# Performance work log

Hardware: AMD Instinct MI355X
Metric: run time of the kernel (lower is better)

The kernel has to match this reference:

```python
import jax, jax.numpy as jnp
import numpy as np

NEG_SLOPE = 0.01  # torch leaky_relu default

def _lrelu(x):
    return jax.nn.leaky_relu(x, NEG_SLOPE)

def _l2norm(x, axis):
    # torch F.normalize(p=2, eps=1e-12)
    n = jnp.linalg.norm(x, axis=axis, keepdims=True)
    return x / jnp.maximum(n, 1e-12)

def setup_inputs() -> dict:
    key = jax.random.key(0)
    ks = jax.random.split(key, 12)
    Nda, Nq, C, Din, Dout = 10000, 64, 1024, 128, 256
    target_adj = (jax.random.uniform(ks[0], (Nda, Nda)) < 0.002).astype(jnp.float32)
    query_adj = (jax.random.uniform(ks[1], (Nq, Nq)) < 0.2).astype(jnp.float32)
    node_features_da = jax.random.normal(ks[2], (Nda, Din), dtype=jnp.float32)
    node_features_q = jax.random.normal(ks[3], (Nq, Din), dtype=jnp.float32)
    candidate_set = jax.random.randint(ks[4], (C,), 0, Nda)
    candidate_adj = (jax.random.uniform(ks[5], (C, C)) < 0.01).astype(jnp.float32)
    s_in = 1.0 / np.sqrt(Din).astype(np.float32)
    s_out = 1.0 / np.sqrt(Dout).astype(np.float32)
    W1_da = jax.random.normal(ks[6], (Din, Dout), dtype=jnp.float32) * s_in
    W1_q = jax.random.normal(ks[7], (Din, Dout), dtype=jnp.float32) * s_in
    W2_da = jax.random.normal(ks[8], (Dout, Dout), dtype=jnp.float32) * s_out
    W2_q = jax.random.normal(ks[9], (Dout, Dout), dtype=jnp.float32) * s_out
    threshold = jnp.float32(0.2)
    return {"target_adj": target_adj, "node_features_da": node_features_da,
            "query_adj": query_adj, "node_features_q": node_features_q,
            "candidate_set": candidate_set, "candidate_adj": candidate_adj,
            "threshold": threshold, "W1_da": W1_da, "W1_q": W1_q,
            "W2_da": W2_da, "W2_q": W2_q}

def _cross_cosine(q, da, candidate_set):
    # cosine similarity between each query node and each candidate target node: [Nq, C]
    return _l2norm(q, 1) @ _l2norm(da[candidate_set], 1).T

def reference(target_adj, node_features_da, query_adj, node_features_q,
              candidate_set, candidate_adj, threshold, W1_da, W1_q, W2_da, W2_q):
    # layer 1: GCN propagation on both graphs (gcn(adj,x) = adj @ x @ W)
    da1 = _lrelu(target_adj @ (node_features_da @ W1_da))   # [Nda, D]
    q1 = _lrelu(query_adj @ (node_features_q @ W1_q))       # [Nq, D]
    c1 = _cross_cosine(q1, da1, candidate_set)               # [Nq, C]
    pre_da1 = da1[candidate_set]                             # [C, D]
    # NOTE: da1[candidate_set].data = ... mutates a temporary in torch -> no-op on da1
    att_da1 = _lrelu(da1)                                    # dropout in eval = identity
    h1_q = c1 @ pre_da1                                      # [Nq, D]
    att_q1 = _lrelu(q1 + _l2norm(h1_q, 0))
    # layer 2
    da2 = _lrelu(target_adj @ (att_da1 @ W2_da))
    q2 = _lrelu(query_adj @ (att_q1 @ W2_q))
    c2 = _cross_cosine(q2, da2, candidate_set)
    pre_da2 = da2[candidate_set]
    att_da2 = _lrelu(da2)                                    # in-place update is again a no-op
    h2_q = c2 @ pre_da2
    att_q2 = _lrelu(q2 + _l2norm(h2_q, 0))
    # graph-level matching score per target node
    emb = jnp.mean(att_q2, axis=0, keepdims=True)            # [1, D]
    num = att_da2 @ emb[0]                                   # [Nda]
    den = jnp.maximum(jnp.linalg.norm(att_da2, axis=1) * jnp.linalg.norm(emb), 1e-8)
    end = (num / den)[None, :]                               # [1, Nda]
    # threshold selection expressed with a mask (jit-safe, same math: excluded
    # rows/cols are zero and do not affect L2 norms, sums, or the trace)
    m = (end[0] > threshold).astype(att_da2.dtype)           # [Nda]
    F_ = att_da2 * m[:, None]
    re_adj = F_ @ F_.T                                       # [Nda, Nda]
    nor_re = _l2norm(re_adj, 1) * target_adj                 # elementwise with original adj
    cnt = jnp.sum(m)
    total = jnp.sum(nor_re)
    tr = jnp.trace(nor_re)
    has = cnt > 0
    pre_avg_degree = jnp.where(has, total / jnp.maximum(cnt, 1.0), 0.0)
    pre_avg_nodes = jnp.where(has, tr, 0.0)
    pre_density = jnp.where(has, 2.0 * total / (tr * (tr - 1.0) + 1e-4), 0.0)
    return (end, att_da2, att_q2, pre_avg_degree, pre_density, pre_avg_nodes)
```

## Files before the change

### kernel.cpp

```cpp
#include <hip/hip_runtime.h>

constexpr int NDA = 10000;
constexpr int NQ  = 64;
constexpr int CND = 1024;
constexpr int DIN = 128;
constexpr int D   = 256;
constexpr int CAP = 96;
constexpr int NB64 = ((NDA + 63) / 64) * (D / 64);
constexpr int GCHUNK = 400;

#define LRELU(x) ((x) >= 0.f ? (x) : 0.01f * (x))

__device__ __forceinline__ float wave_red64(float v) {
#pragma unroll
    for (int o = 32; o; o >>= 1) v += __shfl_down(v, o);
    return v;
}

struct GemmSmem  { float As[32][65]; float Bs[32][68]; };
struct CrossSmem { float qs[D]; float cmw[256]; int sci[256]; float red[4]; float sqn; float part[4][256]; };
struct SpmmSmem  { int sc[CAP]; float part[4][256]; };
struct CsrSmem   { int scnt; };
struct EndSmem   { float se[D]; float scnt; float red[4]; };
struct FinalSmem { int sc[CAP]; float part[4][256]; int n; int sdiag; float r1[4], r2[4], r3[4]; };
struct Attq4Smem { float hbuf[64][65]; float red[4][64]; float invs[64]; };

template <bool RELU_A, bool RELU_C>
__device__ __forceinline__ void gemm_body(GemmSmem& sm, int bx, int by,
                                          const float* __restrict__ A,
                                          const float* __restrict__ B,
                                          float* __restrict__ C,
                                          int M, int N, int K) {
    const int bm = bx * 64, bn = by * 64;
    const int tid = threadIdx.x;
    const int tx = tid & 15, ty = tid >> 4;
    const int lm = tid >> 2, lk = (tid & 3) * 8;
    const int kb = tid >> 3, nb = (tid & 7) * 8;
    const bool aValid = (bm + lm) < M;
    const float* aPtr = A + (size_t)(bm + lm) * K + lk;
    const float* bPtr = B + (size_t)kb * N + bn + nb;
    float4 ra0 = make_float4(0.f, 0.f, 0.f, 0.f), ra1 = ra0, rb0, rb1;
    if (aValid) { ra0 = *(const float4*)aPtr; ra1 = *(const float4*)(aPtr + 4); }
    rb0 = *(const float4*)bPtr;
    rb1 = *(const float4*)(bPtr + 4);
    float acc[4][4] = {};
    for (int k0 = 0; k0 < K; k0 += 32) {
        float4 wa0 = ra0, wa1 = ra1, wb0 = rb0, wb1 = rb1;
        if (RELU_A) {
            wa0.x = LRELU(wa0.x); wa0.y = LRELU(wa0.y); wa0.z = LRELU(wa0.z); wa0.w = LRELU(wa0.w);
            wa1.x = LRELU(wa1.x); wa1.y = LRELU(wa1.y); wa1.z = LRELU(wa1.z); wa1.w = LRELU(wa1.w);
        }
        sm.As[lk + 0][lm] = wa0.x; sm.As[lk + 1][lm] = wa0.y;
        sm.As[lk + 2][lm] = wa0.z; sm.As[lk + 3][lm] = wa0.w;
        sm.As[lk + 4][lm] = wa1.x; sm.As[lk + 5][lm] = wa1.y;
        sm.As[lk + 6][lm] = wa1.z; sm.As[lk + 7][lm] = wa1.w;
        *(float4*)&sm.Bs[kb][nb]     = wb0;
        *(float4*)&sm.Bs[kb][nb + 4] = wb1;
        __syncthreads();
        if (k0 + 32 < K) {
            if (aValid) {
                ra0 = *(const float4*)(aPtr + k0 + 32);
                ra1 = *(const float4*)(aPtr + k0 + 36);
            }
            rb0 = *(const float4*)(bPtr + (size_t)(k0 + 32) * N);
            rb1 = *(const float4*)(bPtr + (size_t)(k0 + 32) * N + 4);
        }
#pragma unroll
        for (int kk = 0; kk < 32; kk++) {
            float av[4], bv[4];
#pragma unroll
            for (int i = 0; i < 4; i++) av[i] = sm.As[kk][ty * 4 + i];
#pragma unroll
            for (int j = 0; j < 4; j++) bv[j] = sm.Bs[kk][tx * 4 + j];
#pragma unroll
            for (int i = 0; i < 4; i++)
#pragma unroll
                for (int j = 0; j < 4; j++) acc[i][j] += av[i] * bv[j];
        }
        __syncthreads();
    }
#pragma unroll
    for (int i = 0; i < 4; i++) {
        int r = bm + ty * 4 + i;
        if (r < M) {
            float4 v = make_float4(acc[i][0], acc[i][1], acc[i][2], acc[i][3]);
            if (RELU_C) { v.x = LRELU(v.x); v.y = LRELU(v.y); v.z = LRELU(v.z); v.w = LRELU(v.w); }
            *(float4*)(C + (size_t)r * N + bn + tx * 4) = v;
        }
    }
}

__device__ __forceinline__ void csr_body(CsrSmem& sm, const float* __restrict__ adj,
                                         int* __restrict__ cols,
                                         int* __restrict__ rowcnt, int row) {
    if (threadIdx.x == 0) sm.scnt = 0;
    __syncthreads();
    const float4* rp = (const float4*)(adj + (size_t)row * NDA);
    for (int i = threadIdx.x; i < NDA / 4; i += 256) {
        float4 v = rp[i];
        if (v.x != 0.f) { int s = atomicAdd(&sm.scnt, 1); if (s < CAP) cols[row * CAP + s] = 4 * i; }
        if (v.y != 0.f) { int s = atomicAdd(&sm.scnt, 1); if (s < CAP) cols[row * CAP + s] = 4 * i + 1; }
        if (v.z != 0.f) { int s = atomicAdd(&sm.scnt, 1); if (s < CAP) cols[row * CAP + s] = 4 * i + 2; }
        if (v.w != 0.f) { int s = atomicAdd(&sm.scnt, 1); if (s < CAP) cols[row * CAP + s] = 4 * i + 3; }
    }
    __syncthreads();
    if (threadIdx.x == 0) rowcnt[row] = min(sm.scnt, CAP);
}

__device__ __forceinline__ void spmm_body(SpmmSmem& sm, const int* __restrict__ cols,
                                          const int* __restrict__ rowcnt,
                                          const float* __restrict__ X,
                                          float* __restrict__ out1,
                                          float* __restrict__ out2, int row) {
    int t = threadIdx.x;
    int w = t >> 6, lane = t & 63;
    int cnt = rowcnt[row];
    if (t < cnt) sm.sc[t] = cols[row * CAP + t];
    __syncthreads();
    float4 acc = make_float4(0.f, 0.f, 0.f, 0.f);
    int k = w;
    for (; k + 4 < cnt; k += 8) {
        const float4* x0 = (const float4*)(X + (size_t)sm.sc[k] * D);
        const float4* x1 = (const float4*)(X + (size_t)sm.sc[k + 4] * D);
        float4 v0 = x0[lane];
        float4 v1 = x1[lane];
        acc.x += v0.x + v1.x; acc.y += v0.y + v1.y;
        acc.z += v0.z + v1.z; acc.w += v0.w + v1.w;
    }
    for (; k < cnt; k += 4) {
        const float4* x0 = (const float4*)(X + (size_t)sm.sc[k] * D);
        float4 v0 = x0[lane];
        acc.x += v0.x; acc.y += v0.y; acc.z += v0.z; acc.w += v0.w;
    }
    *(float4*)&sm.part[w][lane * 4] = acc;
    __syncthreads();
    float s = sm.part[0][t] + sm.part[1][t] + sm.part[2][t] + sm.part[3][t];
    float v = LRELU(s);
    out1[(size_t)row * D + t] = v;
    if (out2) out2[(size_t)row * D + t] = LRELU(v);
}

__device__ __forceinline__ void cross_body(CrossSmem& sm, const float* __restrict__ q,
                                           const float* __restrict__ da,
                                           const int* __restrict__ cand,
                                           float* __restrict__ hpart,
                                           int r, int qr) {
    int t = threadIdx.x;
    int w = t >> 6, lane = t & 63;
    float qv = q[r * D + t];
    sm.qs[t] = qv;
    sm.sci[t] = cand[qr * 256 + t];
    float p = wave_red64(qv * qv);
    if (lane == 0) sm.red[w] = p;
    __syncthreads();
    if (t == 0) sm.sqn = fmaxf(sqrtf(sm.red[0] + sm.red[1] + sm.red[2] + sm.red[3]), 1e-12f);
    __syncthreads();
    float qn = sm.sqn;
    float4 qv4 = *(const float4*)&sm.qs[lane * 4];
    for (int c = w * 64; c < w * 64 + 64; c++) {
        const float4* rp = (const float4*)(da + (size_t)sm.sci[c] * D);
        float4 v = rp[lane];
        float dp = qv4.x * v.x + qv4.y * v.y + qv4.z * v.z + qv4.w * v.w;
        float sq = v.x * v.x + v.y * v.y + v.z * v.z + v.w * v.w;
#pragma unroll
        for (int o = 32; o; o >>= 1) { dp += __shfl_down(dp, o); sq += __shfl_down(sq, o); }
        if (lane == 0) sm.cmw[c] = dp / (qn * fmaxf(sqrtf(sq), 1e-12f));
    }
    __syncthreads();
    float4 acc = make_float4(0.f, 0.f, 0.f, 0.f);
    for (int c = w; c < 256; c += 8) {
        float w0 = sm.cmw[c], w1 = sm.cmw[c + 4];
        const float4* p0 = (const float4*)(da + (size_t)sm.sci[c] * D);
        const float4* p1 = (const float4*)(da + (size_t)sm.sci[c + 4] * D);
        float4 v0 = p0[lane];
        float4 v1 = p1[lane];
        acc.x += w0 * v0.x + w1 * v1.x;
        acc.y += w0 * v0.y + w1 * v1.y;
        acc.z += w0 * v0.z + w1 * v1.z;
        acc.w += w0 * v0.w + w1 * v1.w;
    }
    *(float4*)&sm.part[w][lane * 4] = acc;
    __syncthreads();
    float hs = sm.part[0][t] + sm.part[1][t] + sm.part[2][t] + sm.part[3][t];
    hpart[((size_t)qr * NQ + r) * D + t] = hs;
}

__global__ __launch_bounds__(256) void stage0_kernel(const float* __restrict__ adj,
                                                     int* __restrict__ cols,
                                                     int* __restrict__ rowcnt,
                                                     const float* __restrict__ Fda,
                                                     const float* __restrict__ W1da,
                                                     float* __restrict__ X1,
                                                     const float* __restrict__ Fq,
                                                     const float* __restrict__ W1q,
                                                     float* __restrict__ Xq,
                                                     float* __restrict__ G) {
    __shared__ union { GemmSmem g; CsrSmem z; } sm;
    int bid = blockIdx.x;
    if (bid < NB64) {
        gemm_body<false, false>(sm.g, bid >> 2, bid & 3, Fda, W1da, X1, NDA, D, DIN);
    } else if (bid < NB64 + 4) {
        gemm_body<false, false>(sm.g, 0, bid - NB64, Fq, W1q, Xq, NQ, D, DIN);
    } else if (bid < NB64 + 20) {
        int zb = bid - (NB64 + 4);
        float4* g4 = (float4*)G;
        int base = zb * 1024 + threadIdx.x;
#pragma unroll
        for (int k = 0; k < 4; k++)
            g4[base + k * 256] = make_float4(0.f, 0.f, 0.f, 0.f);
    } else {
        csr_body(sm.z, adj, cols, rowcnt, bid - (NB64 + 20));
    }
}

__global__ __launch_bounds__(256) void stage_sg_kernel(const int* __restrict__ cols,
                                                       const int* __restrict__ rowcnt,
                                                       const float* __restrict__ X,
                                                       float* __restrict__ out1,
                                                       float* __restrict__ out2,
                                                       const float* __restrict__ Aq,
                                                       const float* __restrict__ Bq,
                                                       float* __restrict__ Cq) {
    __shared__ union { GemmSmem g; SpmmSmem s; } sm;
    int bid = blockIdx.x;
    if (bid < 4) {
        gemm_body<false, true>(sm.g, 0, bid, Aq, Bq, Cq, NQ, D, NQ);
    } else {
        spmm_body(sm.s, cols, rowcnt, X, out1, out2, bid - 4);
    }
}

__global__ __launch_bounds__(256) void mergeA_kernel(const float* __restrict__ q1,
                                                     const float* __restrict__ da1,
                                                     const int* __restrict__ cand,
                                                     float* __restrict__ hpart,
                                                     const float* __restrict__ W2da,
                                                     float* __restrict__ Y2) {
    __shared__ union { CrossSmem c; GemmSmem g; } sm;
    int bid = blockIdx.x;
    if (bid < 256) {
        cross_body(sm.c, q1, da1, cand, hpart, bid >> 2, bid & 3);
    } else {
        int t = bid - 256;
        gemm_body<true, false>(sm.g, t >> 2, t & 3, da1, W2da, Y2, NDA, D, D);
    }
}

__global__ __launch_bounds__(256) void cross_kernel(const float* __restrict__ q,
                                                    const float* __restrict__ da,
                                                    const int* __restrict__ cand,
                                                    float* __restrict__ hpart) {
    __shared__ CrossSmem sm;
    cross_body(sm, q, da, cand, hpart, blockIdx.x, blockIdx.y);
}

__global__ __launch_bounds__(256) void qfused_kernel(const float* __restrict__ q,
                                                     const float* __restrict__ hpart,
                                                     const float* __restrict__ W2q,
                                                     float* __restrict__ Zq) {
    __shared__ float aqT[D][65];
    __shared__ float Bs[32][68];
    int d = threadIdx.x;
    float hv[NQ];
    float ss = 0.f;
#pragma unroll
    for (int r = 0; r < NQ; r++) {
        float h = hpart[(size_t)r * D + d]
                + hpart[(size_t)(NQ + r) * D + d]
                + hpart[(size_t)(2 * NQ + r) * D + d]
                + hpart[(size_t)(3 * NQ + r) * D + d];
        hv[r] = h;
        ss += h * h;
    }
    float inv = 1.f / fmaxf(sqrtf(ss), 1e-12f);
#pragma unroll
    for (int r = 0; r < NQ; r++) {
        float v = q[r * D + d] + hv[r] * inv;
        aqT[d][r] = LRELU(v);
    }
    __syncthreads();
    const int bn = blockIdx.x * 64;
    const int tx = d & 15, ty = d >> 4;
    const int kb = d >> 3, nb = (d & 7) * 8;
    float acc[4][4] = {};
    for (int k0 = 0; k0 < D; k0 += 32) {
        float4 b0 = *(const float4*)(W2q + (size_t)(k0 + kb) * D + bn + nb);
        float4 b1 = *(const float4*)(W2q + (size_t)(k0 + kb) * D + bn + nb + 4);
        *(float4*)&Bs[kb][nb]     = b0;
        *(float4*)&Bs[kb][nb + 4] = b1;
        __syncthreads();
#pragma unroll
        for (int kk = 0; kk < 32; kk++) {
            float av[4], bv[4];
#pragma unroll
            for (int i = 0; i < 4; i++) av[i] = aqT[k0 + kk][ty * 4 + i];
#pragma unroll
            for (int j = 0; j < 4; j++) bv[j] = Bs[kk][tx * 4 + j];
#pragma unroll
            for (int i = 0; i < 4; i++)
#pragma unroll
                for (int j = 0; j < 4; j++) acc[i][j] += av[i] * bv[j];
        }
        __syncthreads();
    }
#pragma unroll
    for (int i = 0; i < 4; i++) {
        float4 v = make_float4(acc[i][0], acc[i][1], acc[i][2], acc[i][3]);
        *(float4*)(Zq + (size_t)(ty * 4 + i) * D + bn + tx * 4) = v;
    }
}

__global__ __launch_bounds__(256) void attq4_kernel(const float* __restrict__ q,
                                                    const float* __restrict__ hpart,
                                                    float* __restrict__ attq,
                                                    float* __restrict__ emb,
                                                    float* __restrict__ cnt,
                                                    double* __restrict__ tot,
                                                    double* __restrict__ tr) {
    __shared__ Attq4Smem sm;
    int b = blockIdx.x, t = threadIdx.x;
    int lc = t & 63, rq = t >> 6;
    int c = b * 64 + lc;
    if (b == 0 && t == 0) { *cnt = 0.f; *tot = 0.0; *tr = 0.0; }
    float ss = 0.f;
#pragma unroll
    for (int rr = 0; rr < 16; rr++) {
        int r = rq * 16 + rr;
        float h = hpart[(size_t)r * D + c]
                + hpart[(size_t)(NQ + r) * D + c]
                + hpart[(size_t)(2 * NQ + r) * D + c]
                + hpart[(size_t)(3 * NQ + r) * D + c];
        sm.hbuf[r][lc] = h;
        ss += h * h;
    }
    sm.red[rq][lc] = ss;
    __syncthreads();
    if (rq == 0) {
        float s = sm.red[0][lc] + sm.red[1][lc] + sm.red[2][lc] + sm.red[3][lc];
        sm.invs[lc] = 1.f / fmaxf(sqrtf(s), 1e-12f);
    }
    __syncthreads();
    float inv = sm.invs[lc];
    float es = 0.f;
#pragma unroll
    for (int rr = 0; rr < 16; rr++) {
        int r = rq * 16 + rr;
        float v = q[r * D + c] + sm.hbuf[r][lc] * inv;
        v = LRELU(v);
        attq[r * D + c] = v;
        es += v;
    }
    __syncthreads();
    sm.red[rq][lc] = es;
    __syncthreads();
    if (rq == 0) {
        float e = (sm.red[0][lc] + sm.red[1][lc] + sm.red[2][lc] + sm.red[3][lc]) * (1.f / (float)NQ);
        emb[c] = e;
    }
}

__global__ __launch_bounds__(256) void end_kernel(const float* __restrict__ A,
                                                  const float* __restrict__ emb,
                                                  const float* __restrict__ thr_p,
                                                  float* __restrict__ endv,
                                                  float* __restrict__ m,
                                                  float* __restrict__ cnt) {
    __shared__ EndSmem sm;
    int d = threadIdx.x;
    float ev = emb[d];
    sm.se[d] = ev;
    if (d == 0) sm.scnt = 0.f;
    int w = d >> 6, lane = d & 63;
    float pe = wave_red64(ev * ev);
    if (lane == 0) sm.red[w] = pe;
    __syncthreads();
    float embn = sqrtf(sm.red[0] + sm.red[1] + sm.red[2] + sm.red[3]);
    float thr = *thr_p;
    int row = blockIdx.x * 4 + w;
    const float* ar = A + (size_t)row * D;
    float num = 0.f, sq = 0.f;
#pragma unroll
    for (int s = 0; s < 4; s++) {
        float v = ar[lane + 64 * s];
        num += v * sm.se[lane + 64 * s];
        sq += v * v;
    }
#pragma unroll
    for (int o = 32; o; o >>= 1) { num += __shfl_down(num, o); sq += __shfl_down(sq, o); }
    if (lane == 0) {
        float den = fmaxf(sqrtf(sq) * embn, 1e-8f);
        float e = num / den;
        endv[row] = e;
        float mv = e > thr ? 1.f : 0.f;
        m[row] = mv;
        if (mv != 0.f) atomicAdd(&sm.scnt, 1.f);
    }
    __syncthreads();
    if (d == 0 && sm.scnt != 0.f) atomicAdd(cnt, sm.scnt);
}

__global__ __launch_bounds__(256) void G_kernel(const float* __restrict__ A,
                                                const float* __restrict__ m,
                                                float* __restrict__ G) {
    __shared__ float SA[8][64], SB[8][64];
    int ti = blockIdx.x >> 2, tj = blockIdx.x & 3;
    int base = blockIdx.y * GCHUNK;
    int tid = threadIdx.x;
    int tx = tid & 15, ty = tid >> 4;
    float acc[4][4] = {};
    for (int g0 = 0; g0 < GCHUNK; g0 += 8) {
        for (int l = tid; l < 512; l += 256) {
            int rr = l >> 6, c = l & 63;
            int r = base + g0 + rr;
            float mv = m[r];
            SA[rr][c] = A[(size_t)r * D + ti * 64 + c] * mv;
            SB[rr][c] = A[(size_t)r * D + tj * 64 + c];
        }
        __syncthreads();
#pragma unroll
        for (int rr = 0; rr < 8; rr++) {
            float av[4], bv[4];
#pragma unroll
            for (int i = 0; i < 4; i++) av[i] = SA[rr][ty * 4 + i];
#pragma unroll
            for (int j = 0; j < 4; j++) bv[j] = SB[rr][tx * 4 + j];
#pragma unroll
            for (int i = 0; i < 4; i++)
#pragma unroll
                for (int j = 0; j < 4; j++) acc[i][j] += av[i] * bv[j];
        }
        __syncthreads();
    }
#pragma unroll
    for (int i = 0; i < 4; i++)
#pragma unroll
        for (int j = 0; j < 4; j++)
            atomicAdd(&G[(ti * 64 + ty * 4 + i) * D + tj * 64 + tx * 4 + j], acc[i][j]);
}

__global__ __launch_bounds__(256) void gemmH_kernel(const float* __restrict__ A,
                                                    const float* __restrict__ B,
                                                    float* __restrict__ C) {
    __shared__ GemmSmem sm;
    gemm_body<false, false>(sm, blockIdx.x, blockIdx.y, A, B, C, NDA, D, D);
}

__global__ __launch_bounds__(256) void final_kernel(const int* __restrict__ cols,
                                                    const int* __restrict__ rowcnt,
                                                    const float* __restrict__ m,
                                                    const float* __restrict__ A,
                                                    const float* __restrict__ H,
                                                    double* __restrict__ total,
                                                    double* __restrict__ tr) {
    int i = blockIdx.x;
    if (m[i] == 0.f) return;
    __shared__ FinalSmem sm;
    int t = threadIdx.x;
    int w = t >> 6, lane = t & 63;
    int cnt = rowcnt[i];
    if (t == 0) { sm.n = 0; sm.sdiag = 0; }
    __syncthreads();
    if (t < cnt) {
        int j = cols[i * CAP + t];
        if (m[j] != 0.f) {
            int s = atomicAdd(&sm.n, 1);
            sm.sc[s] = j;
            if (j == i) sm.sdiag = 1;
        }
    }
    __syncthreads();
    int n = sm.n;
    float4 acc = make_float4(0.f, 0.f, 0.f, 0.f);
    int k = w;
    for (; k + 4 < n; k += 8) {
        const float4* x0 = (const float4*)(A + (size_t)sm.sc[k] * D);
        const float4* x1 = (const float4*)(A + (size_t)sm.sc[k + 4] * D);
        float4 v0 = x0[lane];
        float4 v1 = x1[lane];
        acc.x += v0.x + v1.x; acc.y += v0.y + v1.y;
        acc.z += v0.z + v1.z; acc.w += v0.w + v1.w;
    }
    for (; k < n; k += 4) {
        const float4* x0 = (const float4*)(A + (size_t)sm.sc[k] * D);
        float4 v0 = x0[lane];
        acc.x += v0.x; acc.y += v0.y; acc.z += v0.z; acc.w += v0.w;
    }
    *(float4*)&sm.part[w][lane * 4] = acc;
    __syncthreads();
    float av = A[(size_t)i * D + t];
    float hv = H[(size_t)i * D + t];
    float sd = sm.part[0][t] + sm.part[1][t] + sm.part[2][t] + sm.part[3][t];
    float p1 = av * sd, p2 = av * hv, p3 = av * av;
#pragma unroll
    for (int o = 32; o; o >>= 1) {
        p1 += __shfl_down(p1, o);
        p2 += __shfl_down(p2, o);
        p3 += __shfl_down(p3, o);
    }
    if (lane == 0) { sm.r1[w] = p1; sm.r2[w] = p2; sm.r3[w] = p3; }
    __syncthreads();
    if (t == 0) {
        float num  = sm.r1[0] + sm.r1[1] + sm.r1[2] + sm.r1[3];
        float den2 = sm.r2[0] + sm.r2[1] + sm.r2[2] + sm.r2[3];
        float self = sm.r3[0] + sm.r3[1] + sm.r3[2] + sm.r3[3];
        float denom = fmaxf(sqrtf(den2), 1e-12f);
        double inv = 1.0 / (double)denom;
        if (num != 0.f) atomicAdd(total, (double)num * inv);
        if (sm.sdiag) atomicAdd(tr, (double)self * inv);
    }
}

__global__ void scalars_kernel(const float* __restrict__ cnt,
                               const double* __restrict__ total,
                               const double* __restrict__ tr,
                               float* __restrict__ out) {
    float c = *cnt;
    float T = (float)*total;
    float R = (float)*tr;
    bool has = c > 0.f;
    out[0] = has ? (T / fmaxf(c, 1.f)) : 0.f;
    out[1] = has ? (2.f * T / (R * (R - 1.f) + 1e-4f)) : 0.f;
    out[2] = has ? R : 0.f;
}

extern "C" void kernel_launch(void* const* d_in, const int* in_sizes, int n_in,
                              void* d_out, int out_size, void* d_ws, size_t ws_size,
                              hipStream_t stream) {
    (void)in_sizes; (void)n_in; (void)out_size; (void)ws_size;
    const float* adj  = (const float*)d_in[0];
    const float* Fda  = (const float*)d_in[1];
    const float* Qadj = (const float*)d_in[2];
    const float* Fq   = (const float*)d_in[3];
    const int*   cand = (const int*)d_in[4];
    const float* thr  = (const float*)d_in[6];
    const float* W1da = (const float*)d_in[7];
    const float* W1q  = (const float*)d_in[8];
    const float* W2da = (const float*)d_in[9];
    const float* W2q  = (const float*)d_in[10];

    float* out = (float*)d_out;
    float* o_end    = out;
    float* o_attda2 = out + NDA;
    float* o_attq2  = out + NDA + (size_t)NDA * D;
    float* o_sc     = o_attq2 + NQ * D;

    char* w = (char*)d_ws;
    size_t off = 0;
    auto alloc = [&](size_t b) { size_t r = off; off += (b + 255) & ~(size_t)255; return r; };
    float* bufA = (float*)(w + alloc((size_t)NDA * D * 4));
    float* bufB = (float*)(w + alloc((size_t)NDA * D * 4));
    float* bufC = (float*)(w + alloc((size_t)NDA * D * 4));
    int* colsb   = (int*)(w + alloc((size_t)NDA * CAP * 4));
    int* rowcntb = (int*)(w + alloc((size_t)NDA * 4));
    float* mbuf  = (float*)(w + alloc((size_t)NDA * 4));
    float* Gb    = (float*)(w + alloc((size_t)D * D * 4));
    char* zbase = w + alloc(256);
    float* cntb  = (float*)zbase;
    double* totb = (double*)(zbase + 8);
    double* trb  = (double*)(zbase + 16);
    float* xq   = (float*)(w + alloc((size_t)NQ * D * 4));
    float* q1b  = (float*)(w + alloc((size_t)NQ * D * 4));
    float* q2b  = (float*)(w + alloc((size_t)NQ * D * 4));
    float* hpart = (float*)(w + alloc((size_t)4 * NQ * D * 4));
    float* embb = (float*)(w + alloc((size_t)(D + 1) * 4));

    stage0_kernel<<<NB64 + 20 + NDA, 256, 0, stream>>>(adj, colsb, rowcntb,
                                                       Fda, W1da, bufA, Fq, W1q, xq, Gb);
    stage_sg_kernel<<<NDA + 4, 256, 0, stream>>>(colsb, rowcntb, bufA, bufB, (float*)nullptr,
                                                 Qadj, xq, q1b);
    mergeA_kernel<<<256 + NB64, 256, 0, stream>>>(q1b, bufB, cand, hpart, W2da, bufA);
    qfused_kernel<<<4, 256, 0, stream>>>(q1b, hpart, W2q, xq);
    stage_sg_kernel<<<NDA + 4, 256, 0, stream>>>(colsb, rowcntb, bufA, bufC, o_attda2,
                                                 Qadj, xq, q2b);
    cross_kernel<<<dim3(NQ, 4), 256, 0, stream>>>(q2b, bufC, cand, hpart);
    attq4_kernel<<<4, 256, 0, stream>>>(q2b, hpart, o_attq2, embb, cntb, totb, trb);
    end_kernel<<<NDA / 4, 256, 0, stream>>>(o_attda2, embb, thr, o_end, mbuf, cntb);
    G_kernel<<<dim3(16, NDA / GCHUNK), 256, 0, stream>>>(o_attda2, mbuf, Gb);
    gemmH_kernel<<<dim3((NDA + 63) / 64, D / 64), 256, 0, stream>>>(o_attda2, Gb, bufB);
    final_kernel<<<NDA, 256, 0, stream>>>(colsb, rowcntb, mbuf, o_attda2, bufB, totb, trb);
    scalars_kernel<<<1, 1, 0, stream>>>(cntb, totb, trb, o_sc);
}
```

Before: 1.078 ms.

## Fuse end-score and Gram kernels; unroll sparse gathers by four

Merges end_kernel and G_kernel into one launch. The Gram blocks recompute the end-score mask for their own row chunk, so they no longer wait on a separate end_kernel pass. The sparse row-gather loops in spmm and final now issue four row loads per iteration instead of two, giving more memory parallelism. The cost is redundant score computation: each of the 16 tiles per chunk recomputes the mask for all 400 rows. The fused kernel also uses more shared memory per block.

```diff
diff --git a/kernel.cpp b/kernel.cpp
--- a/kernel.cpp
+++ b/kernel.cpp
@@ -8,6 +8,7 @@
 constexpr int CAP = 96;
 constexpr int NB64 = ((NDA + 63) / 64) * (D / 64);
 constexpr int GCHUNK = 400;
+constexpr int NGB = 16 * (NDA / GCHUNK);
 
 #define LRELU(x) ((x) >= 0.f ? (x) : 0.01f * (x))
 
@@ -15,15 +16,31 @@
 #pragma unroll
     for (int o = 32; o; o >>= 1) v += __shfl_down(v, o);
     return v;
+}
+
+__device__ __noinline__ float end_score(const float* __restrict__ ar,
+                                        const float* se, float embn, int lane) {
+    float num = 0.f, sq = 0.f;
+#pragma unroll
+    for (int s = 0; s < 4; s++) {
+        float v = ar[lane + 64 * s];
+        num += v * se[lane + 64 * s];
+        sq += v * v;
+    }
+#pragma unroll
+    for (int o = 32; o; o >>= 1) { num += __shfl_down(num, o); sq += __shfl_down(sq, o); }
+    float den = fmaxf(sqrtf(sq) * embn, 1e-8f);
+    return num / den;
 }
 
 struct GemmSmem  { float As[32][65]; float Bs[32][68]; };
 struct CrossSmem { float qs[D]; float cmw[256]; int sci[256]; float red[4]; float sqn; float part[4][256]; };
 struct SpmmSmem  { int sc[CAP]; float part[4][256]; };
 struct CsrSmem   { int scnt; };
-struct EndSmem   { float se[D]; float scnt; float red[4]; };
 struct FinalSmem { int sc[CAP]; float part[4][256]; int n; int sdiag; float r1[4], r2[4], r3[4]; };
 struct Attq4Smem { float hbuf[64][65]; float red[4][64]; float invs[64]; };
+struct GSm  { float SA[8][64]; float SB[8][64]; float se[256]; float red[4]; float mrow[GCHUNK]; };
+struct ESm  { float se[256]; float scnt; float red[4]; };
 
 template <bool RELU_A, bool RELU_C>
 __device__ __forceinline__ void gemm_body(GemmSmem& sm, int bx, int by,
@@ -119,17 +136,18 @@
     __syncthreads();
     float4 acc = make_float4(0.f, 0.f, 0.f, 0.f);
     int k = w;
-    for (; k + 4 < cnt; k += 8) {
-        const float4* x0 = (const float4*)(X + (size_t)sm.sc[k] * D);
-        const float4* x1 = (const float4*)(X + (size_t)sm.sc[k + 4] * D);
-        float4 v0 = x0[lane];
-        float4 v1 = x1[lane];
-        acc.x += v0.x + v1.x; acc.y += v0.y + v1.y;
-        acc.z += v0.z + v1.z; acc.w += v0.w + v1.w;
+    for (; k + 12 < cnt; k += 16) {
+        float4 v0 = ((const float4*)(X + (size_t)sm.sc[k]      * D))[lane];
+        float4 v1 = ((const float4*)(X + (size_t)sm.sc[k + 4]  * D))[lane];
+        float4 v2 = ((const float4*)(X + (size_t)sm.sc[k + 8]  * D))[lane];
+        float4 v3 = ((const float4*)(X + (size_t)sm.sc[k + 12] * D))[lane];
+        acc.x += (v0.x + v1.x) + (v2.x + v3.x);
+        acc.y += (v0.y + v1.y) + (v2.y + v3.y);
+        acc.z += (v0.z + v1.z) + (v2.z + v3.z);
+        acc.w += (v0.w + v1.w) + (v2.w + v3.w);
     }
     for (; k < cnt; k += 4) {
-        const float4* x0 = (const float4*)(X + (size_t)sm.sc[k] * D);
-        float4 v0 = x0[lane];
+        float4 v0 = ((const float4*)(X + (size_t)sm.sc[k] * D))[lane];
         acc.x += v0.x; acc.y += v0.y; acc.z += v0.z; acc.w += v0.w;
     }
     *(float4*)&sm.part[w][lane * 4] = acc;
@@ -359,83 +377,86 @@
     }
 }
 
-__global__ __launch_bounds__(256) void end_kernel(const float* __restrict__ A,
-                                                  const float* __restrict__ emb,
-                                                  const float* __restrict__ thr_p,
-                                                  float* __restrict__ endv,
-                                                  float* __restrict__ m,
-                                                  float* __restrict__ cnt) {
-    __shared__ EndSmem sm;
-    int d = threadIdx.x;
-    float ev = emb[d];
-    sm.se[d] = ev;
-    if (d == 0) sm.scnt = 0.f;
-    int w = d >> 6, lane = d & 63;
-    float pe = wave_red64(ev * ev);
-    if (lane == 0) sm.red[w] = pe;
-    __syncthreads();
-    float embn = sqrtf(sm.red[0] + sm.red[1] + sm.red[2] + sm.red[3]);
-    float thr = *thr_p;
-    int row = blockIdx.x * 4 + w;
-    const float* ar = A + (size_t)row * D;
-    float num = 0.f, sq = 0.f;
-#pragma unroll
-    for (int s = 0; s < 4; s++) {
-        float v = ar[lane + 64 * s];
-        num += v * sm.se[lane + 64 * s];
-        sq += v * v;
-    }
-#pragma unroll
-    for (int o = 32; o; o >>= 1) { num += __shfl_down(num, o); sq += __shfl_down(sq, o); }
-    if (lane == 0) {
-        float den = fmaxf(sqrtf(sq) * embn, 1e-8f);
-        float e = num / den;
-        endv[row] = e;
-        float mv = e > thr ? 1.f : 0.f;
-        m[row] = mv;
-        if (mv != 0.f) atomicAdd(&sm.scnt, 1.f);
-    }
-    __syncthreads();
-    if (d == 0 && sm.scnt != 0.f) atomicAdd(cnt, sm.scnt);
-}
-
-__global__ __launch_bounds__(256) void G_kernel(const float* __restrict__ A,
-                                                const float* __restrict__ m,
-                                                float* __restrict__ G) {
-    __shared__ float SA[8][64], SB[8][64];
-    int ti = blockIdx.x >> 2, tj = blockIdx.x & 3;
-    int base = blockIdx.y * GCHUNK;
-    int tid = threadIdx.x;
-    int tx = tid & 15, ty = tid >> 4;
-    float acc[4][4] = {};
-    for (int g0 = 0; g0 < GCHUNK; g0 += 8) {
-        for (int l = tid; l < 512; l += 256) {
-            int rr = l >> 6, c = l & 63;
-            int r = base + g0 + rr;
-            float mv = m[r];
-            SA[rr][c] = A[(size_t)r * D + ti * 64 + c] * mv;
-            SB[rr][c] = A[(size_t)r * D + tj * 64 + c];
-        }
-        __syncthreads();
-#pragma unroll
-        for (int rr = 0; rr < 8; rr++) {
-            float av[4], bv[4];
-#pragma unroll
-            for (int i = 0; i < 4; i++) av[i] = SA[rr][ty * 4 + i];
-#pragma unroll
-            for (int j = 0; j < 4; j++) bv[j] = SB[rr][tx * 4 + j];
-#pragma unroll
-            for (int i = 0; i < 4; i++)
-#pragma unroll
-                for (int j = 0; j < 4; j++) acc[i][j] += av[i] * bv[j];
-        }
-        __syncthreads();
-    }
-#pragma unroll
-    for (int i = 0; i < 4; i++)
-#pragma unroll
-        for (int j = 0; j < 4; j++)
-            atomicAdd(&G[(ti * 64 + ty * 4 + i) * D + tj * 64 + tx * 4 + j], acc[i][j]);
+__global__ __launch_bounds__(256) void endG_kernel(const float* __restrict__ A,
+                                                   const float* __restrict__ emb,
+                                                   const float* __restrict__ thr_p,
+                                                   float* __restrict__ endv,
+                                                   float* __restrict__ m,
+                                                   float* __restrict__ cnt,
+                                                   float* __restrict__ G) {
+    __shared__ union { GSm g; ESm e; } sm;
+    int bid = blockIdx.x;
+    int t = threadIdx.x;
+    int w = t >> 6, lane = t & 63;
+    if (bid < NGB) {
+        int tile = bid & 15, chunk = bid >> 4;
+        int ti = tile >> 2, tj = tile & 3;
+        int base = chunk * GCHUNK;
+        float ev = emb[t];
+        sm.g.se[t] = ev;
+        float pe = wave_red64(ev * ev);
+        if (lane == 0) sm.g.red[w] = pe;
+        __syncthreads();
+        float embn = sqrtf(sm.g.red[0] + sm.g.red[1] + sm.g.red[2] + sm.g.red[3]);
+        float thr = *thr_p;
+        for (int rr = w; rr < GCHUNK; rr += 4) {
+            const float* ar = A + (size_t)(base + rr) * D;
+            float e = end_score(ar, sm.g.se, embn, lane);
+            if (lane == 0) sm.g.mrow[rr] = e > thr ? 1.f : 0.f;
+        }
+        __syncthreads();
+        int tx = t & 15, ty = t >> 4;
+        float acc[4][4] = {};
+        for (int g0 = 0; g0 < GCHUNK; g0 += 8) {
+            for (int l = t; l < 512; l += 256) {
+                int rr = l >> 6, c = l & 63;
+                int r = base + g0 + rr;
+                float mv = sm.g.mrow[g0 + rr];
+                sm.g.SA[rr][c] = A[(size_t)r * D + ti * 64 + c] * mv;
+                sm.g.SB[rr][c] = A[(size_t)r * D + tj * 64 + c];
+            }
+            __syncthreads();
+#pragma unroll
+            for (int rr = 0; rr < 8; rr++) {
+                float av[4], bv[4];
+#pragma unroll
+                for (int i = 0; i < 4; i++) av[i] = sm.g.SA[rr][ty * 4 + i];
+#pragma unroll
+                for (int j = 0; j < 4; j++) bv[j] = sm.g.SB[rr][tx * 4 + j];
+#pragma unroll
+                for (int i = 0; i < 4; i++)
+#pragma unroll
+                    for (int j = 0; j < 4; j++) acc[i][j] += av[i] * bv[j];
+            }
+            __syncthreads();
+        }
+#pragma unroll
+        for (int i = 0; i < 4; i++)
+#pragma unroll
+            for (int j = 0; j < 4; j++)
+                atomicAdd(&G[(ti * 64 + ty * 4 + i) * D + tj * 64 + tx * 4 + j], acc[i][j]);
+    } else {
+        int quad = bid - NGB;
+        float ev = emb[t];
+        sm.e.se[t] = ev;
+        if (t == 0) sm.e.scnt = 0.f;
+        float pe = wave_red64(ev * ev);
+        if (lane == 0) sm.e.red[w] = pe;
+        __syncthreads();
+        float embn = sqrtf(sm.e.red[0] + sm.e.red[1] + sm.e.red[2] + sm.e.red[3]);
+        float thr = *thr_p;
+        int row = quad * 4 + w;
+        const float* ar = A + (size_t)row * D;
+        float e = end_score(ar, sm.e.se, embn, lane);
+        if (lane == 0) {
+            endv[row] = e;
+            float mv = e > thr ? 1.f : 0.f;
+            m[row] = mv;
+            if (mv != 0.f) atomicAdd(&sm.e.scnt, 1.f);
+        }
+        __syncthreads();
+        if (t == 0 && sm.e.scnt != 0.f) atomicAdd(cnt, sm.e.scnt);
+    }
 }
 
 __global__ __launch_bounds__(256) void gemmH_kernel(const float* __restrict__ A,
@@ -472,17 +493,18 @@
     int n = sm.n;
     float4 acc = make_float4(0.f, 0.f, 0.f, 0.f);
     int k = w;
-    for (; k + 4 < n; k += 8) {
-        const float4* x0 = (const float4*)(A + (size_t)sm.sc[k] * D);
-        const float4* x1 = (const float4*)(A + (size_t)sm.sc[k + 4] * D);
-        float4 v0 = x0[lane];
-        float4 v1 = x1[lane];
-        acc.x += v0.x + v1.x; acc.y += v0.y + v1.y;
-        acc.z += v0.z + v1.z; acc.w += v0.w + v1.w;
+    for (; k + 12 < n; k += 16) {
+        float4 v0 = ((const float4*)(A + (size_t)sm.sc[k]      * D))[lane];
+        float4 v1 = ((const float4*)(A + (size_t)sm.sc[k + 4]  * D))[lane];
+        float4 v2 = ((const float4*)(A + (size_t)sm.sc[k + 8]  * D))[lane];
+        float4 v3 = ((const float4*)(A + (size_t)sm.sc[k + 12] * D))[lane];
+        acc.x += (v0.x + v1.x) + (v2.x + v3.x);
+        acc.y += (v0.y + v1.y) + (v2.y + v3.y);
+        acc.z += (v0.z + v1.z) + (v2.z + v3.z);
+        acc.w += (v0.w + v1.w) + (v2.w + v3.w);
     }
     for (; k < n; k += 4) {
-        const float4* x0 = (const float4*)(A + (size_t)sm.sc[k] * D);
-        float4 v0 = x0[lane];
+        float4 v0 = ((const float4*)(A + (size_t)sm.sc[k] * D))[lane];
         acc.x += v0.x; acc.y += v0.y; acc.z += v0.z; acc.w += v0.w;
     }
     *(float4*)&sm.part[w][lane * 4] = acc;
@@ -574,8 +596,7 @@
                                                  Qadj, xq, q2b);
     cross_kernel<<<dim3(NQ, 4), 256, 0, stream>>>(q2b, bufC, cand, hpart);
     attq4_kernel<<<4, 256, 0, stream>>>(q2b, hpart, o_attq2, embb, cntb, totb, trb);
-    end_kernel<<<NDA / 4, 256, 0, stream>>>(o_attda2, embb, thr, o_end, mbuf, cntb);
-    G_kernel<<<dim3(16, NDA / GCHUNK), 256, 0, stream>>>(o_attda2, mbuf, Gb);
+    endG_kernel<<<NGB + NDA / 4, 256, 0, stream>>>(o_attda2, embb, thr, o_end, mbuf, cntb, Gb);
     gemmH_kernel<<<dim3((NDA + 63) / 64, D / 64), 256, 0, stream>>>(o_attda2, Gb, bufB);
     final_kernel<<<NDA, 256, 0, stream>>>(colsb, rowcntb, mbuf, o_attda2, bufB, totb, trb);
     scalars_kernel<<<1, 1, 0, stream>>>(cntb, totb, trb, o_sc);
```

New measurement: 1.138 ms. 1.06x slower.
